# Kernel optimization log

Hardware: AMD Instinct MI355X
Metric: run time of the kernel (lower is better)

Reference implementation:

```python
import jax, jax.numpy as jnp
import numpy as np


def setup_inputs() -> dict:
    key = jax.random.key(0)
    k1, k2, k3 = jax.random.split(key, 3)
    B, S, I, H, M = 8, 2048, 256, 256, 1024
    x = jax.random.normal(k1, (B, S, I), dtype=jnp.float32)
    mem = jax.random.normal(k2, (B, M, H), dtype=jnp.float32)
    # Xavier-uniform with gain=sqrt(2): bound = sqrt(2)*sqrt(6/(H+I))
    bound = np.sqrt(2.0) * np.sqrt(6.0 / (H + I))
    W = jax.random.uniform(k3, (H, I), dtype=jnp.float32, minval=-bound, maxval=bound)
    return {"x": x, "mem": mem, "W": W}


def reference(x, mem, W):
    # key[b,s,h] = relu(sum_i x[b,s,i] * W[h,i])  -- one batched GEMM for all t
    key_seq = jax.nn.relu(jnp.einsum("bsi,hi->bsh", x, W))
    # val[b,s,m] = sum_h key[b,s,h] * mem[b,m,h]
    val_seq = jnp.einsum("bsh,bmh->bsm", key_seq, mem)
    return key_seq, val_seq
```

## Files before the change

kernel.cpp:

```cpp
#include <hip/hip_runtime.h>
#include <cstdint>

typedef unsigned short u16;
typedef __bf16 bf16x8 __attribute__((ext_vector_type(8)));
typedef float f32x4 __attribute__((ext_vector_type(4)));
typedef u16 u16x8 __attribute__((ext_vector_type(8)));

#define NX 4194304L
#define NW 65536L
#define NM 2097152L
#define WS_MEM (NW)
#define WS_KEY (NW + NM)

__device__ __forceinline__ u16 f2bf_rne(float f) {
  union { float f; uint32_t u; } v; v.f = f;
  uint32_t r = v.u + 0x7fffu + ((v.u >> 16) & 1u);
  return (u16)(r >> 16);
}

__device__ __forceinline__ u16x8 cvt8(float4 a, float4 b) {
  u16x8 o;
  o[0]=f2bf_rne(a.x); o[1]=f2bf_rne(a.y); o[2]=f2bf_rne(a.z); o[3]=f2bf_rne(a.w);
  o[4]=f2bf_rne(b.x); o[5]=f2bf_rne(b.y); o[6]=f2bf_rne(b.z); o[7]=f2bf_rne(b.w);
  return o;
}

__global__ void convert_bf16_kernel(const float* __restrict__ mem,
                                    const float* __restrict__ W,
                                    u16* __restrict__ ws) {
  long e = ((long)blockIdx.x * blockDim.x + threadIdx.x) * 8;
  if (e >= NW + NM) return;
  const float* src; long l;
  if (e < NW) { src = W;   l = e; }
  else        { src = mem; l = e - NW; }
  float4 f0 = *(const float4*)(src + l);
  float4 f1 = *(const float4*)(src + l + 4);
  *(u16x8*)(ws + e) = cvt8(f0, f1);
}

#define G1_BM 64
#define G1_BN 128
#define BK 32

__global__ __launch_bounds__(256, 2)
void gemm1_x(const float* __restrict__ x, const u16* __restrict__ Wb,
             float* __restrict__ key_f, u16* __restrict__ key_bf)
{
  const int K = 256, N = 256;
  __shared__ __align__(16) u16 sA[2][G1_BM * BK];
  __shared__ __align__(16) u16 sB[2][G1_BN * BK];
  const int tid  = threadIdx.x;
  const int wave = tid >> 6;
  const int lane = tid & 63;
  const int quad = lane >> 4;
  const int r    = lane & 15;
  const int wm   = wave >> 1;
  const int wn   = wave & 1;

  const int gx  = gridDim.x;
  const int nwg = gx * (int)gridDim.y;
  const int id  = (int)blockIdx.x + gx * (int)blockIdx.y;
  const int cpx = nwg >> 3;
  const int lid = (id & 7) * cpx + (id >> 3);
  const int bm  = (lid / gx) * G1_BM;
  const int bn  = (lid % gx) * G1_BN;

  const long ldr = (long)K * 2;

  f32x4 acc[2][4];
  #pragma unroll
  for (int i = 0; i < 2; i++)
    #pragma unroll
    for (int j = 0; j < 4; j++)
      acc[i][j] = f32x4{0.f, 0.f, 0.f, 0.f};

  const int o0 = wave * 1024 + lane * 16;
  auto stageB = [&](int buf, int kt) {
    #pragma unroll
    for (int rr = 0; rr < 2; rr++) {
      const int o    = rr * 4096 + o0;
      const int row  = o >> 6;
      const int colb = o & 63;
      const char* g = (const char*)Wb + (long)(bn + row) * ldr + (long)kt * 2 + colb;
      char* l = (char*)&sB[buf][0] + rr * 4096 + wave * 1024;
      __builtin_amdgcn_global_load_lds((const __attribute__((address_space(1))) void*)g,
                                       (__attribute__((address_space(3))) void*)l, 16, 0, 0);
    }
  };

  float4 xa[2];
  const int arow = tid >> 2;
  const int ac0  = (tid & 3) * 8;
  auto loadA = [&](int kt) {
    const float* g = x + (long)(bm + arow) * K + kt + ac0;
    xa[0] = *(const float4*)g;
    xa[1] = *(const float4*)(g + 4);
  };
  auto writeA = [&](int buf) {
    *(u16x8*)&sA[buf][arow * BK + ac0] = cvt8(xa[0], xa[1]);
  };

  loadA(0); writeA(0);
  stageB(0, 0);
  __syncthreads();

  const int NT = K / BK;
  for (int t = 0; t < NT; ++t) {
    const int cur = t & 1, nxt = cur ^ 1;
    const bool pf = (t + 1 < NT);
    if (pf) {
      loadA((t + 1) * BK);
      stageB(nxt, (t + 1) * BK);
    }

    bf16x8 af[2], bfr[4];
    #pragma unroll
    for (int i = 0; i < 2; i++)
      af[i] = *(const bf16x8*)&sA[cur][(wm * 32 + i * 16 + r) * BK + quad * 8];
    #pragma unroll
    for (int j = 0; j < 4; j++)
      bfr[j] = *(const bf16x8*)&sB[cur][(wn * 64 + j * 16 + r) * BK + quad * 8];
    #pragma unroll
    for (int i = 0; i < 2; i++)
      #pragma unroll
      for (int j = 0; j < 4; j++)
        acc[i][j] = __builtin_amdgcn_mfma_f32_16x16x32_bf16(af[i], bfr[j], acc[i][j], 0, 0, 0);

    if (pf) writeA(nxt);
    __syncthreads();
  }

  #pragma unroll
  for (int i = 0; i < 2; i++) {
    #pragma unroll
    for (int j = 0; j < 4; j++) {
      #pragma unroll
      for (int reg = 0; reg < 4; reg++) {
        const int row = bm + wm * 32 + i * 16 + quad * 4 + reg;
        const int col = bn + wn * 64 + j * 16 + r;
        float v = acc[i][j][reg];
        v = v > 0.f ? v : 0.f;
        const long idx = (long)row * N + col;
        key_f[idx]  = v;
        key_bf[idx] = f2bf_rne(v);
      }
    }
  }
}

#define BM 128
#define BN 128

__global__ __launch_bounds__(256, 3)
void gemm2(const u16* __restrict__ A, const u16* __restrict__ B,
           float* __restrict__ C,
           int M, int N, int K,
           long sA_batch, long sB_batch, long sC_batch)
{
  __shared__ __align__(16) u16 sA[2][BM * BK];
  __shared__ __align__(16) u16 sB[2][BN * BK];
  const int tid  = threadIdx.x;
  const int wave = tid >> 6;
  const int lane = tid & 63;
  const int quad = lane >> 4;
  const int r    = lane & 15;
  const int wm   = wave >> 1;
  const int wn   = wave & 1;

  const int gx  = gridDim.x, gy = gridDim.y;
  const int nwg = gx * gy * (int)gridDim.z;
  const int id  = (int)blockIdx.x + gx * ((int)blockIdx.y + gy * (int)blockIdx.z);
  const int cpx = nwg >> 3;
  const int lid = (id & 7) * cpx + (id >> 3);
  const int bx  = lid % gx;
  const int tq  = lid / gx;
  const int by  = tq % gy;
  const int bz  = tq / gy;

  const int bm    = by * BM;
  const int bn    = bx * BN;
  const int batch = bz;

  const char* Ab = (const char*)(A + (long)batch * sA_batch);
  const char* Bb = (const char*)(B + (long)batch * sB_batch);
  const long ldr = (long)K * 2;

  f32x4 acc[4][4];
  #pragma unroll
  for (int i = 0; i < 4; i++)
    #pragma unroll
    for (int j = 0; j < 4; j++)
      acc[i][j] = f32x4{0.f, 0.f, 0.f, 0.f};

  const int o0 = wave * 1024 + lane * 16;
  auto stage = [&](u16* dst, const char* src, int kt) {
    #pragma unroll
    for (int rr = 0; rr < 2; rr++) {
      const int o    = rr * 4096 + o0;
      const int row  = o >> 6;
      const int colb = o & 63;
      const char* g = src + (long)row * ldr + (long)kt * 2 + colb;
      char* l = (char*)dst + rr * 4096 + wave * 1024;
      __builtin_amdgcn_global_load_lds((const __attribute__((address_space(1))) void*)g,
                                       (__attribute__((address_space(3))) void*)l, 16, 0, 0);
    }
  };

  stage(&sA[0][0], Ab + (long)bm * ldr, 0);
  stage(&sB[0][0], Bb + (long)bn * ldr, 0);
  __syncthreads();

  const int NT = K / BK;
  for (int t = 0; t < NT; ++t) {
    const int cur = t & 1, nxt = cur ^ 1;
    const bool pf = (t + 1 < NT);
    if (pf) {
      stage(&sA[nxt][0], Ab + (long)bm * ldr, (t + 1) * BK);
      stage(&sB[nxt][0], Bb + (long)bn * ldr, (t + 1) * BK);
    }

    bf16x8 af[4], bfr[4];
    #pragma unroll
    for (int i = 0; i < 4; i++)
      af[i] = *(const bf16x8*)&sA[cur][(wm * 64 + i * 16 + r) * BK + quad * 8];
    #pragma unroll
    for (int j = 0; j < 4; j++)
      bfr[j] = *(const bf16x8*)&sB[cur][(wn * 64 + j * 16 + r) * BK + quad * 8];
    #pragma unroll
    for (int i = 0; i < 4; i++)
      #pragma unroll
      for (int j = 0; j < 4; j++)
        acc[i][j] = __builtin_amdgcn_mfma_f32_16x16x32_bf16(af[i], bfr[j], acc[i][j], 0, 0, 0);

    __syncthreads();
  }

  float* Co = C + (long)batch * sC_batch;
  #pragma unroll
  for (int i = 0; i < 4; i++) {
    #pragma unroll
    for (int j = 0; j < 4; j++) {
      #pragma unroll
      for (int reg = 0; reg < 4; reg++) {
        const int row = bm + wm * 64 + i * 16 + quad * 4 + reg;
        const int col = bn + wn * 64 + j * 16 + r;
        Co[(long)row * N + col] = acc[i][j][reg];
      }
    }
  }
}

extern "C" void kernel_launch(void* const* d_in, const int* in_sizes, int n_in,
                              void* d_out, int out_size, void* d_ws, size_t ws_size,
                              hipStream_t stream) {
  const float* x   = (const float*)d_in[0];
  const float* mem = (const float*)d_in[1];
  const float* W   = (const float*)d_in[2];
  float* out   = (float*)d_out;
  float* key_f = out;
  float* val_f = out + NX;
  u16* ws     = (u16*)d_ws;
  u16* W_bf   = ws;
  u16* mem_bf = ws + WS_MEM;
  u16* key_bf = ws + WS_KEY;

  convert_bf16_kernel<<<(int)((NW + NM) / 8 / 256), 256, 0, stream>>>(mem, W, ws);

  dim3 g1(256 / G1_BN, 16384 / G1_BM, 1);
  gemm1_x<<<g1, 256, 0, stream>>>(x, W_bf, key_f, key_bf);

  dim3 g2(1024 / BN, 2048 / BM, 8);
  gemm2<<<g2, 256, 0, stream>>>(key_bf, mem_bf, val_f,
                                2048, 1024, 256,
                                (long)2048 * 256, (long)1024 * 256,
                                (long)2048 * 1024);
}
```

Measured before the change: 124.7 us.

## Triple-buffer gemm2 with vmcnt-based waits and smaller 128x64 tiles

Gemm2 moves from double-buffered 128x128 tiles to triple-buffered 128x64 tiles. It prefetches two K-steps ahead and replaces __syncthreads with explicit s_waitcnt vmcnt plus s_barrier, so the barrier waits only on the oldest stage's async LDS loads. The smaller tile doubles the workgroup count and raises the occupancy target to 4, aiming to hide global latency better. The cost is less operand reuse per tile and a hand-counted vmcnt that is fragile if the load count changes.

New measurement: 126.5 us. About the same (+1.4%).

```diff
diff --git a/kernel.cpp b/kernel.cpp
--- a/kernel.cpp
+++ b/kernel.cpp
@@ -67,13 +67,6 @@
 
   const long ldr = (long)K * 2;
 
-  f32x4 acc[2][4];
-  #pragma unroll
-  for (int i = 0; i < 2; i++)
-    #pragma unroll
-    for (int j = 0; j < 4; j++)
-      acc[i][j] = f32x4{0.f, 0.f, 0.f, 0.f};
-
   const int o0 = wave * 1024 + lane * 16;
   auto stageB = [&](int buf, int kt) {
     #pragma unroll
@@ -100,6 +93,13 @@
     *(u16x8*)&sA[buf][arow * BK + ac0] = cvt8(xa[0], xa[1]);
   };
 
+  f32x4 acc[2][4];
+  #pragma unroll
+  for (int i = 0; i < 2; i++)
+    #pragma unroll
+    for (int j = 0; j < 4; j++)
+      acc[i][j] = f32x4{0.f, 0.f, 0.f, 0.f};
+
   loadA(0); writeA(0);
   stageB(0, 0);
   __syncthreads();
@@ -112,7 +112,6 @@
       loadA((t + 1) * BK);
       stageB(nxt, (t + 1) * BK);
     }
-
     bf16x8 af[2], bfr[4];
     #pragma unroll
     for (int i = 0; i < 2; i++)
@@ -125,7 +124,6 @@
       #pragma unroll
       for (int j = 0; j < 4; j++)
         acc[i][j] = __builtin_amdgcn_mfma_f32_16x16x32_bf16(af[i], bfr[j], acc[i][j], 0, 0, 0);
-
     if (pf) writeA(nxt);
     __syncthreads();
   }
@@ -148,17 +146,18 @@
   }
 }
 
-#define BM 128
-#define BN 128
-
-__global__ __launch_bounds__(256, 3)
+#define G2_BM 128
+#define G2_BN 64
+#define NBUF 3
+
+__global__ __launch_bounds__(256, 4)
 void gemm2(const u16* __restrict__ A, const u16* __restrict__ B,
            float* __restrict__ C,
            int M, int N, int K,
            long sA_batch, long sB_batch, long sC_batch)
 {
-  __shared__ __align__(16) u16 sA[2][BM * BK];
-  __shared__ __align__(16) u16 sB[2][BN * BK];
+  __shared__ __align__(16) u16 sA[NBUF][G2_BM * BK];
+  __shared__ __align__(16) u16 sB[NBUF][G2_BN * BK];
   const int tid  = threadIdx.x;
   const int wave = tid >> 6;
   const int lane = tid & 63;
@@ -177,73 +176,86 @@
   const int by  = tq % gy;
   const int bz  = tq / gy;
 
-  const int bm    = by * BM;
-  const int bn    = bx * BN;
+  const int bm    = by * G2_BM;
+  const int bn    = bx * G2_BN;
   const int batch = bz;
 
-  const char* Ab = (const char*)(A + (long)batch * sA_batch);
-  const char* Bb = (const char*)(B + (long)batch * sB_batch);
+  const char* Asrc = (const char*)(A + (long)batch * sA_batch) + (long)bm * ((long)K * 2);
+  const char* Bsrc = (const char*)(B + (long)batch * sB_batch) + (long)bn * ((long)K * 2);
   const long ldr = (long)K * 2;
 
-  f32x4 acc[4][4];
-  #pragma unroll
-  for (int i = 0; i < 4; i++)
-    #pragma unroll
-    for (int j = 0; j < 4; j++)
-      acc[i][j] = f32x4{0.f, 0.f, 0.f, 0.f};
-
   const int o0 = wave * 1024 + lane * 16;
-  auto stage = [&](u16* dst, const char* src, int kt) {
+  auto stageA = [&](int buf, int kt) {
     #pragma unroll
     for (int rr = 0; rr < 2; rr++) {
       const int o    = rr * 4096 + o0;
       const int row  = o >> 6;
       const int colb = o & 63;
-      const char* g = src + (long)row * ldr + (long)kt * 2 + colb;
-      char* l = (char*)dst + rr * 4096 + wave * 1024;
+      const char* g = Asrc + (long)row * ldr + (long)kt * 2 + colb;
+      char* l = (char*)&sA[buf][0] + rr * 4096 + wave * 1024;
       __builtin_amdgcn_global_load_lds((const __attribute__((address_space(1))) void*)g,
                                        (__attribute__((address_space(3))) void*)l, 16, 0, 0);
     }
   };
-
-  stage(&sA[0][0], Ab + (long)bm * ldr, 0);
-  stage(&sB[0][0], Bb + (long)bn * ldr, 0);
-  __syncthreads();
+  auto stageB = [&](int buf, int kt) {
+    const int row  = o0 >> 6;
+    const int colb = o0 & 63;
+    const char* g = Bsrc + (long)row * ldr + (long)kt * 2 + colb;
+    char* l = (char*)&sB[buf][0] + wave * 1024;
+    __builtin_amdgcn_global_load_lds((const __attribute__((address_space(1))) void*)g,
+                                     (__attribute__((address_space(3))) void*)l, 16, 0, 0);
+  };
+
+  f32x4 acc[4][2];
+  #pragma unroll
+  for (int i = 0; i < 4; i++)
+    #pragma unroll
+    for (int j = 0; j < 2; j++)
+      acc[i][j] = f32x4{0.f, 0.f, 0.f, 0.f};
+
+  stageA(0, 0);  stageB(0, 0);
+  stageA(1, BK); stageB(1, BK);
+  asm volatile("s_waitcnt vmcnt(3)" ::: "memory");
+  __builtin_amdgcn_s_barrier();
+  __builtin_amdgcn_sched_barrier(0);
 
   const int NT = K / BK;
   for (int t = 0; t < NT; ++t) {
-    const int cur = t & 1, nxt = cur ^ 1;
-    const bool pf = (t + 1 < NT);
-    if (pf) {
-      stage(&sA[nxt][0], Ab + (long)bm * ldr, (t + 1) * BK);
-      stage(&sB[nxt][0], Bb + (long)bn * ldr, (t + 1) * BK);
-    }
-
-    bf16x8 af[4], bfr[4];
+    const int cur = t % 3;
+    if (t + 2 < NT) {
+      const int nb = (t + 2) % 3;
+      stageA(nb, (t + 2) * BK);
+      stageB(nb, (t + 2) * BK);
+    }
+    bf16x8 af[4], bfr[2];
     #pragma unroll
     for (int i = 0; i < 4; i++)
       af[i] = *(const bf16x8*)&sA[cur][(wm * 64 + i * 16 + r) * BK + quad * 8];
     #pragma unroll
-    for (int j = 0; j < 4; j++)
-      bfr[j] = *(const bf16x8*)&sB[cur][(wn * 64 + j * 16 + r) * BK + quad * 8];
+    for (int j = 0; j < 2; j++)
+      bfr[j] = *(const bf16x8*)&sB[cur][(wn * 32 + j * 16 + r) * BK + quad * 8];
     #pragma unroll
     for (int i = 0; i < 4; i++)
       #pragma unroll
-      for (int j = 0; j < 4; j++)
+      for (int j = 0; j < 2; j++)
         acc[i][j] = __builtin_amdgcn_mfma_f32_16x16x32_bf16(af[i], bfr[j], acc[i][j], 0, 0, 0);
-
-    __syncthreads();
+    if (t + 1 < NT) {
+      if (t + 2 < NT) asm volatile("s_waitcnt vmcnt(3)" ::: "memory");
+      else            asm volatile("s_waitcnt vmcnt(0)" ::: "memory");
+      __builtin_amdgcn_s_barrier();
+      __builtin_amdgcn_sched_barrier(0);
+    }
   }
 
   float* Co = C + (long)batch * sC_batch;
   #pragma unroll
   for (int i = 0; i < 4; i++) {
     #pragma unroll
-    for (int j = 0; j < 4; j++) {
+    for (int j = 0; j < 2; j++) {
       #pragma unroll
       for (int reg = 0; reg < 4; reg++) {
         const int row = bm + wm * 64 + i * 16 + quad * 4 + reg;
-        const int col = bn + wn * 64 + j * 16 + r;
+        const int col = bn + wn * 32 + j * 16 + r;
         Co[(long)row * N + col] = acc[i][j][reg];
       }
     }
@@ -269,7 +281,7 @@
   dim3 g1(256 / G1_BN, 16384 / G1_BM, 1);
   gemm1_x<<<g1, 256, 0, stream>>>(x, W_bf, key_f, key_bf);
 
-  dim3 g2(1024 / BN, 2048 / BM, 8);
+  dim3 g2(1024 / G2_BN, 2048 / G2_BM, 8);
   gemm2<<<g2, 256, 0, stream>>>(key_bf, mem_bf, val_f,
                                 2048, 1024, 256,
                                 (long)2048 * 256, (long)1024 * 256,
```

## Fuse mem conversion into GEMM1 launch and triple-buffer GEMM2 pipeline

Applied to the files above, without the earlier changes.

Removes the separate conversion kernel. The fp32 to bf16 conversion of mem now runs in extra trailing blocks of the first GEMM launch, and W is converted on the fly inside GEMM1 from fp32 through registers. GEMM2 moves from double to triple buffering with explicit vmcnt waits and raw barriers, so two tiles are in flight and there is one barrier per iteration. This saves one launch and overlaps loads better, at the cost of more LDS per block (which may reduce occupancy) and redundant W conversion across blocks.

Result: no change. 125.1 us (+0.3%).

```diff
diff --git a/kernel.cpp b/kernel.cpp
--- a/kernel.cpp
+++ b/kernel.cpp
@@ -7,10 +7,7 @@
 typedef u16 u16x8 __attribute__((ext_vector_type(8)));
 
 #define NX 4194304L
-#define NW 65536L
 #define NM 2097152L
-#define WS_MEM (NW)
-#define WS_KEY (NW + NM)
 
 __device__ __forceinline__ u16 f2bf_rne(float f) {
   union { float f; uint32_t u; } v; v.f = f;
@@ -25,31 +22,31 @@
   return o;
 }
 
-__global__ void convert_bf16_kernel(const float* __restrict__ mem,
-                                    const float* __restrict__ W,
-                                    u16* __restrict__ ws) {
-  long e = ((long)blockIdx.x * blockDim.x + threadIdx.x) * 8;
-  if (e >= NW + NM) return;
-  const float* src; long l;
-  if (e < NW) { src = W;   l = e; }
-  else        { src = mem; l = e - NW; }
-  float4 f0 = *(const float4*)(src + l);
-  float4 f1 = *(const float4*)(src + l + 4);
-  *(u16x8*)(ws + e) = cvt8(f0, f1);
-}
-
 #define G1_BM 64
 #define G1_BN 128
 #define BK 32
+#define G1_BLOCKS 512
 
 __global__ __launch_bounds__(256, 2)
-void gemm1_x(const float* __restrict__ x, const u16* __restrict__ Wb,
-             float* __restrict__ key_f, u16* __restrict__ key_bf)
+void g1_fused(const float* __restrict__ x, const float* __restrict__ W,
+              const float* __restrict__ mem,
+              float* __restrict__ key_f, u16* __restrict__ key_bf,
+              u16* __restrict__ mem_bf)
 {
+  const int bid = blockIdx.x;
+  const int tid = threadIdx.x;
+
+  if (bid >= G1_BLOCKS) {
+    long e = ((long)(bid - G1_BLOCKS) * 256 + tid) * 8;
+    float4 f0 = *(const float4*)(mem + e);
+    float4 f1 = *(const float4*)(mem + e + 4);
+    *(u16x8*)(mem_bf + e) = cvt8(f0, f1);
+    return;
+  }
+
   const int K = 256, N = 256;
   __shared__ __align__(16) u16 sA[2][G1_BM * BK];
   __shared__ __align__(16) u16 sB[2][G1_BN * BK];
-  const int tid  = threadIdx.x;
   const int wave = tid >> 6;
   const int lane = tid & 63;
   const int quad = lane >> 4;
@@ -57,36 +54,10 @@
   const int wm   = wave >> 1;
   const int wn   = wave & 1;
 
-  const int gx  = gridDim.x;
-  const int nwg = gx * (int)gridDim.y;
-  const int id  = (int)blockIdx.x + gx * (int)blockIdx.y;
-  const int cpx = nwg >> 3;
-  const int lid = (id & 7) * cpx + (id >> 3);
-  const int bm  = (lid / gx) * G1_BM;
-  const int bn  = (lid % gx) * G1_BN;
-
-  const long ldr = (long)K * 2;
-
-  f32x4 acc[2][4];
-  #pragma unroll
-  for (int i = 0; i < 2; i++)
-    #pragma unroll
-    for (int j = 0; j < 4; j++)
-      acc[i][j] = f32x4{0.f, 0.f, 0.f, 0.f};
-
-  const int o0 = wave * 1024 + lane * 16;
-  auto stageB = [&](int buf, int kt) {
-    #pragma unroll
-    for (int rr = 0; rr < 2; rr++) {
-      const int o    = rr * 4096 + o0;
-      const int row  = o >> 6;
-      const int colb = o & 63;
-      const char* g = (const char*)Wb + (long)(bn + row) * ldr + (long)kt * 2 + colb;
-      char* l = (char*)&sB[buf][0] + rr * 4096 + wave * 1024;
-      __builtin_amdgcn_global_load_lds((const __attribute__((address_space(1))) void*)g,
-                                       (__attribute__((address_space(3))) void*)l, 16, 0, 0);
-    }
-  };
+  const int cpx = G1_BLOCKS >> 3;
+  const int lid = (bid & 7) * cpx + (bid >> 3);
+  const int bm  = (lid >> 1) * G1_BM;
+  const int bn  = (lid & 1) * G1_BN;
 
   float4 xa[2];
   const int arow = tid >> 2;
@@ -100,8 +71,29 @@
     *(u16x8*)&sA[buf][arow * BK + ac0] = cvt8(xa[0], xa[1]);
   };
 
-  loadA(0); writeA(0);
-  stageB(0, 0);
+  float4 xb[4];
+  const int brow = tid >> 1;
+  const int bc0  = (tid & 1) * 16;
+  auto loadB = [&](int kt) {
+    const float* g = W + (long)(bn + brow) * K + kt + bc0;
+    #pragma unroll
+    for (int c = 0; c < 4; c++) xb[c] = *(const float4*)(g + c * 4);
+  };
+  auto writeB = [&](int buf) {
+    u16* d = &sB[buf][brow * BK + bc0];
+    *(u16x8*)d       = cvt8(xb[0], xb[1]);
+    *(u16x8*)(d + 8) = cvt8(xb[2], xb[3]);
+  };
+
+  f32x4 acc[2][4];
+  #pragma unroll
+  for (int i = 0; i < 2; i++)
+    #pragma unroll
+    for (int j = 0; j < 4; j++)
+      acc[i][j] = f32x4{0.f, 0.f, 0.f, 0.f};
+
+  loadA(0); loadB(0);
+  writeA(0); writeB(0);
   __syncthreads();
 
   const int NT = K / BK;
@@ -110,9 +102,8 @@
     const bool pf = (t + 1 < NT);
     if (pf) {
       loadA((t + 1) * BK);
-      stageB(nxt, (t + 1) * BK);
-    }
-
+      loadB((t + 1) * BK);
+    }
     bf16x8 af[2], bfr[4];
     #pragma unroll
     for (int i = 0; i < 2; i++)
@@ -125,8 +116,10 @@
       #pragma unroll
       for (int j = 0; j < 4; j++)
         acc[i][j] = __builtin_amdgcn_mfma_f32_16x16x32_bf16(af[i], bfr[j], acc[i][j], 0, 0, 0);
-
-    if (pf) writeA(nxt);
+    if (pf) {
+      writeA(nxt);
+      writeB(nxt);
+    }
     __syncthreads();
   }
 
@@ -148,8 +141,9 @@
   }
 }
 
-#define BM 128
-#define BN 128
+#define G2_BM 128
+#define G2_BN 128
+#define NBUF 3
 
 __global__ __launch_bounds__(256, 3)
 void gemm2(const u16* __restrict__ A, const u16* __restrict__ B,
@@ -157,8 +151,8 @@
            int M, int N, int K,
            long sA_batch, long sB_batch, long sC_batch)
 {
-  __shared__ __align__(16) u16 sA[2][BM * BK];
-  __shared__ __align__(16) u16 sB[2][BN * BK];
+  __shared__ __align__(16) u16 sA[NBUF][G2_BM * BK];
+  __shared__ __align__(16) u16 sB[NBUF][G2_BN * BK];
   const int tid  = threadIdx.x;
   const int wave = tid >> 6;
   const int lane = tid & 63;
@@ -177,20 +171,13 @@
   const int by  = tq % gy;
   const int bz  = tq / gy;
 
-  const int bm    = by * BM;
-  const int bn    = bx * BN;
+  const int bm    = by * G2_BM;
+  const int bn    = bx * G2_BN;
   const int batch = bz;
 
-  const char* Ab = (const char*)(A + (long)batch * sA_batch);
-  const char* Bb = (const char*)(B + (long)batch * sB_batch);
   const long ldr = (long)K * 2;
-
-  f32x4 acc[4][4];
-  #pragma unroll
-  for (int i = 0; i < 4; i++)
-    #pragma unroll
-    for (int j = 0; j < 4; j++)
-      acc[i][j] = f32x4{0.f, 0.f, 0.f, 0.f};
+  const char* Asrc = (const char*)(A + (long)batch * sA_batch) + (long)bm * ldr;
+  const char* Bsrc = (const char*)(B + (long)batch * sB_batch) + (long)bn * ldr;
 
   const int o0 = wave * 1024 + lane * 16;
   auto stage = [&](u16* dst, const char* src, int kt) {
@@ -206,19 +193,27 @@
     }
   };
 
-  stage(&sA[0][0], Ab + (long)bm * ldr, 0);
-  stage(&sB[0][0], Bb + (long)bn * ldr, 0);
-  __syncthreads();
+  f32x4 acc[4][4];
+  #pragma unroll
+  for (int i = 0; i < 4; i++)
+    #pragma unroll
+    for (int j = 0; j < 4; j++)
+      acc[i][j] = f32x4{0.f, 0.f, 0.f, 0.f};
+
+  stage(&sA[0][0], Asrc, 0);  stage(&sB[0][0], Bsrc, 0);
+  stage(&sA[1][0], Asrc, BK); stage(&sB[1][0], Bsrc, BK);
+  asm volatile("s_waitcnt vmcnt(4)" ::: "memory");
+  __builtin_amdgcn_s_barrier();
+  __builtin_amdgcn_sched_barrier(0);
 
   const int NT = K / BK;
   for (int t = 0; t < NT; ++t) {
-    const int cur = t & 1, nxt = cur ^ 1;
-    const bool pf = (t + 1 < NT);
-    if (pf) {
-      stage(&sA[nxt][0], Ab + (long)bm * ldr, (t + 1) * BK);
-      stage(&sB[nxt][0], Bb + (long)bn * ldr, (t + 1) * BK);
-    }
-
+    const int cur = t % 3;
+    if (t + 2 < NT) {
+      const int nb = (t + 2) % 3;
+      stage(&sA[nb][0], Asrc, (t + 2) * BK);
+      stage(&sB[nb][0], Bsrc, (t + 2) * BK);
+    }
     bf16x8 af[4], bfr[4];
     #pragma unroll
     for (int i = 0; i < 4; i++)
@@ -231,8 +226,12 @@
       #pragma unroll
       for (int j = 0; j < 4; j++)
         acc[i][j] = __builtin_amdgcn_mfma_f32_16x16x32_bf16(af[i], bfr[j], acc[i][j], 0, 0, 0);
-
-    __syncthreads();
+    if (t + 1 < NT) {
+      if (t + 2 < NT) asm volatile("s_waitcnt vmcnt(4)" ::: "memory");
+      else            asm volatile("s_waitcnt vmcnt(0)" ::: "memory");
+      __builtin_amdgcn_s_barrier();
+      __builtin_amdgcn_sched_barrier(0);
+    }
   }
 
   float* Co = C + (long)batch * sC_batch;
@@ -260,16 +259,13 @@
   float* key_f = out;
   float* val_f = out + NX;
   u16* ws     = (u16*)d_ws;
-  u16* W_bf   = ws;
-  u16* mem_bf = ws + WS_MEM;
-  u16* key_bf = ws + WS_KEY;
-
-  convert_bf16_kernel<<<(int)((NW + NM) / 8 / 256), 256, 0, stream>>>(mem, W, ws);
-
-  dim3 g1(256 / G1_BN, 16384 / G1_BM, 1);
-  gemm1_x<<<g1, 256, 0, stream>>>(x, W_bf, key_f, key_bf);
-
-  dim3 g2(1024 / BN, 2048 / BM, 8);
+  u16* mem_bf = ws;
+  u16* key_bf = ws + NM;
+
+  g1_fused<<<G1_BLOCKS + (int)(NM / 2048), 256, 0, stream>>>(
+      x, W, mem, key_f, key_bf, mem_bf);
+
+  dim3 g2(1024 / G2_BN, 2048 / G2_BM, 8);
   gemm2<<<g2, 256, 0, stream>>>(key_bf, mem_bf, val_f,
                                 2048, 1024, 256,
                                 (long)2048 * 256, (long)1024 * 256,
```
